# Optimization experiments

Hardware: AMD Instinct MI355X
Metric: run time of the kernel (lower is better)

Reference implementation:

```python
import jax, jax.numpy as jnp
import numpy as np

N_NODES = 100000
N_REL = 4
N_EDGES = 400000
IN_F, H_F, OUT_F = 128, 128, 64


def setup_inputs() -> dict:
    key = jax.random.key(0)
    ks = jax.random.split(key, 7)
    x = jax.random.normal(ks[0], (N_NODES, IN_F), dtype=jnp.float32)
    src_idx = jax.random.randint(ks[1], (N_REL, N_EDGES), 0, N_NODES, dtype=jnp.int64)
    dst_idx = jax.random.randint(ks[2], (N_REL, N_EDGES), 0, N_NODES, dtype=jnp.int64)
    # Glorot-ish scale for the per-relation GraphConv weights
    W1 = jax.random.normal(ks[3], (N_REL, IN_F, H_F), dtype=jnp.float32) * (1.0 / np.sqrt(IN_F))
    b1 = jnp.zeros((N_REL, H_F), dtype=jnp.float32)
    W2 = jax.random.normal(ks[4], (N_REL, H_F, OUT_F), dtype=jnp.float32) * (1.0 / np.sqrt(H_F))
    b2 = jnp.zeros((N_REL, OUT_F), dtype=jnp.float32)
    return {"x": x, "src_idx": src_idx, "dst_idx": dst_idx,
            "W1": W1, "b1": b1, "W2": W2, "b2": b2}


def _graph_conv(x, src, dst, W, b):
    """DGL GraphConv with norm='both': out = D_in^{-1/2} A^T D_out^{-1/2} x W + b."""
    n = x.shape[0]
    ones = jnp.ones(src.shape[0], dtype=x.dtype)
    deg_out = jnp.maximum(jax.ops.segment_sum(ones, src, num_segments=n), 1.0)
    deg_in = jnp.maximum(jax.ops.segment_sum(ones, dst, num_segments=n), 1.0)
    xn = x * jax.lax.rsqrt(deg_out)[:, None]              # [N, F] src-side norm
    msg = jnp.take(xn, src, axis=0)                        # [E, F] gather
    agg = jax.ops.segment_sum(msg, dst, num_segments=n)   # [N, F] scatter-add
    agg = agg * jax.lax.rsqrt(deg_in)[:, None]            # dst-side norm
    return agg @ W + b


def _hetero_layer(x, src_idx, dst_idx, Ws, bs):
    # per-relation conv, sum-aggregated across relations (HeteroGraphConv 'sum')
    per_rel = jax.vmap(lambda s, d, W, b: _graph_conv(x, s, d, W, b))(src_idx, dst_idx, Ws, bs)
    return per_rel.sum(axis=0)


def reference(x, src_idx, dst_idx, W1, b1, W2, b2):
    h = jax.nn.relu(_hetero_layer(x, src_idx, dst_idx, W1, b1))
    return _hetero_layer(h, src_idx, dst_idx, W2, b2)
```

## Files before the change

kernel.cpp:

```cpp
#include <hip/hip_runtime.h>
#include <hip/hip_bf16.h>

#define NN 100000
#define NR 4
#define NE 400000
#define INF 128
#define HF 128
#define OUTF 64

#define WIN 16384
#define WIN2 (WIN / 2)
#define NWIN 7
#define SUB 16
#define SLICE (NE / SUB)

typedef __attribute__((ext_vector_type(8))) short s16x8;
typedef __attribute__((ext_vector_type(4))) float f32x4;

__global__ __launch_bounds__(256) void deg_win_kernel(const int* __restrict__ src,
                                                      const int* __restrict__ dst,
                                                      unsigned int* __restrict__ parts) {
    __shared__ unsigned int hist[WIN2];
    int arr = blockIdx.z;
    int r   = blockIdx.y;
    int win = blockIdx.x / SUB;
    int sub = blockIdx.x % SUB;
    const int4* idx4 = (const int4*)((arr ? dst : src) + (size_t)r * NE + (size_t)sub * SLICE);
    int base = win * WIN;

    uint4 z4 = make_uint4(0, 0, 0, 0);
    for (int i = threadIdx.x; i < WIN2 / 4; i += 256) ((uint4*)hist)[i] = z4;
    __syncthreads();

    auto proc = [&](int4 v) {
        int a;
        a = v.x - base; if ((unsigned)a < WIN) atomicAdd(&hist[a >> 1], 1u << ((a & 1) << 4));
        a = v.y - base; if ((unsigned)a < WIN) atomicAdd(&hist[a >> 1], 1u << ((a & 1) << 4));
        a = v.z - base; if ((unsigned)a < WIN) atomicAdd(&hist[a >> 1], 1u << ((a & 1) << 4));
        a = v.w - base; if ((unsigned)a < WIN) atomicAdd(&hist[a >> 1], 1u << ((a & 1) << 4));
    };

    constexpr int NV = SLICE / 4;
    int i = threadIdx.x;
    for (; i + 256 < NV; i += 512) {
        int4 va = idx4[i];
        int4 vb = idx4[i + 256];
        proc(va);
        proc(vb);
    }
    if (i < NV) proc(idx4[i]);
    __syncthreads();

    unsigned int* outp = parts + ((((size_t)arr * NR + r) * NWIN + win) * SUB + sub) * WIN2;
    for (int j = threadIdx.x; j < WIN2 / 4; j += 256)
        ((uint4*)outp)[j] = ((const uint4*)hist)[j];
}

__global__ void red_norm_kernel(const unsigned int* __restrict__ parts, int* __restrict__ deg_tot,
                                float* __restrict__ rno, float* __restrict__ rni) {
    int n = blockIdx.x * blockDim.x + threadIdx.x;
    if (n >= NN) return;
    int win = n / WIN, off = n % WIN;
    int word = off >> 1, sh = (off & 1) << 4;
    int tot = 0;
    #pragma unroll
    for (int r = 0; r < NR; r++) {
        const unsigned int* p0 = parts + (((size_t)0 * NR + r) * NWIN + win) * SUB * WIN2 + word;
        const unsigned int* p1 = parts + (((size_t)1 * NR + r) * NWIN + win) * SUB * WIN2 + word;
        int so = 0, si = 0;
        #pragma unroll
        for (int s = 0; s < SUB; s++) {
            so += (p0[(size_t)s * WIN2] >> sh) & 0xFFFFu;
            si += (p1[(size_t)s * WIN2] >> sh) & 0xFFFFu;
        }
        rno[(size_t)r * NN + n] = rsqrtf(fmaxf((float)so, 1.0f));
        rni[(size_t)r * NN + n] = rsqrtf(fmaxf((float)si, 1.0f));
        tot += si;
    }
    deg_tot[n] = tot;
}

__global__ void scan_block_kernel(const int* __restrict__ in, int* __restrict__ out,
                                  int* __restrict__ blockSums, int n) {
    __shared__ int sd[256];
    int t = threadIdx.x;
    int base = blockIdx.x * 1024 + t * 4;
    int v[4];
    #pragma unroll
    for (int j = 0; j < 4; j++) v[j] = (base + j < n) ? in[base + j] : 0;
    int ts = v[0] + v[1] + v[2] + v[3];
    sd[t] = ts;
    __syncthreads();
    int acc = ts;
    for (int off = 1; off < 256; off <<= 1) {
        int x = (t >= off) ? sd[t - off] : 0;
        __syncthreads();
        acc += x; sd[t] = acc;
        __syncthreads();
    }
    int run = acc - ts;
    #pragma unroll
    for (int j = 0; j < 4; j++) {
        if (base + j < n) out[base + j] = run;
        run += v[j];
    }
    if (t == 255) blockSums[blockIdx.x] = acc;
}

__global__ void scan_sums_kernel(int* __restrict__ blockSums, int nb) {
    __shared__ int sd[512];
    int t = threadIdx.x;
    int v = (t < nb) ? blockSums[t] : 0;
    sd[t] = v;
    __syncthreads();
    int acc = v;
    for (int off = 1; off < 512; off <<= 1) {
        int x = (t >= off) ? sd[t - off] : 0;
        __syncthreads();
        acc += x; sd[t] = acc;
        __syncthreads();
    }
    if (t < nb) blockSums[t] = acc - v;
}

__global__ void scan_add_kernel(int* __restrict__ row_ptr, const int* __restrict__ blockSums,
                                int* __restrict__ cursor, int n) {
    int i = blockIdx.x * blockDim.x + threadIdx.x;
    if (i < n) {
        int v = row_ptr[i] + blockSums[i >> 10];
        row_ptr[i] = v;
        cursor[i] = v;
    }
    if (i == 0) row_ptr[n] = NR * NE;
}

__global__ void csr_build_kernel(const int* __restrict__ src, const int* __restrict__ dst,
                                 const float* __restrict__ rno, const float* __restrict__ rni,
                                 int* __restrict__ cursor, int2* __restrict__ edges) {
    int r = blockIdx.y;
    int i = blockIdx.x * blockDim.x + threadIdx.x;
    if (i >= NE) return;
    int s = src[(size_t)r * NE + i];
    int d = dst[(size_t)r * NE + i];
    int pos = atomicAdd(&cursor[d], 1);
    float c = rno[(size_t)r * NN + s] * rni[(size_t)r * NN + d];
    edges[pos] = make_int2(r * NN + s, __float_as_int(c));
}

__global__ void bsum_kernel(const float* __restrict__ b1, const float* __restrict__ b2,
                            float* __restrict__ bsum1, float* __restrict__ bsum2) {
    int t = threadIdx.x;
    if (t < HF) {
        float s = 0.f;
        for (int r = 0; r < NR; r++) s += b1[r * HF + t];
        bsum1[t] = s;
    } else if (t < HF + OUTF) {
        int f = t - HF;
        float s = 0.f;
        for (int r = 0; r < NR; r++) s += b2[r * OUTF + f];
        bsum2[f] = s;
    }
}

__global__ void conv_w_kernel(const float* __restrict__ W1, const float* __restrict__ W2,
                              __hip_bfloat16* __restrict__ Wt1, __hip_bfloat16* __restrict__ Wt2) {
    int id = blockIdx.x * blockDim.x + threadIdx.x;
    if (id < NR * HF * INF) {
        int r = id >> 14, rem = id & 16383;
        int n_ = rem >> 7, k = rem & 127;
        Wt1[id] = __float2bfloat16(W1[((size_t)r * INF + k) * HF + n_]);
    } else {
        int id2 = id - NR * HF * INF;
        if (id2 < NR * OUTF * HF) {
            int r = id2 >> 13, rem = id2 & 8191;
            int n_ = rem >> 7, k = rem & 127;
            Wt2[id2] = __float2bfloat16(W2[((size_t)r * HF + k) * OUTF + n_]);
        }
    }
}

__device__ __forceinline__ s16x8 pack_bf16x8(float4 a0, float4 a1) {
    union { s16x8 v; __hip_bfloat162 h[4]; } u;
    u.h[0] = __float22bfloat162_rn(make_float2(a0.x, a0.y));
    u.h[1] = __float22bfloat162_rn(make_float2(a0.z, a0.w));
    u.h[2] = __float22bfloat162_rn(make_float2(a1.x, a1.y));
    u.h[3] = __float22bfloat162_rn(make_float2(a1.z, a1.w));
    return u.v;
}

__device__ __forceinline__ void load_lds_16(const void* g, void* l) {
    __builtin_amdgcn_global_load_lds(
        (const __attribute__((address_space(1))) void*)g,
        (__attribute__((address_space(3))) void*)l, 16, 0, 0);
}

template<int F, typename AT>
__global__ __launch_bounds__(256, 3) void gemm_all(const AT* __restrict__ Xb,
                                                   const __hip_bfloat16* __restrict__ Wt,
                                                   __hip_bfloat16* __restrict__ Zb, int nrel) {
    constexpr int NT = F / 16;
    constexpr int NG = F * 16;
    __shared__ __attribute__((aligned(16))) __hip_bfloat16 Bs[F * 128];

    int tid  = threadIdx.x;
    int wid  = tid >> 6;
    int lane = tid & 63;
    int quad = lane >> 4;
    int l16  = lane & 15;
    int sw   = l16 & 7;

    int mbase = blockIdx.x * 128;

    int bofs[4];
    #pragma unroll
    for (int kb = 0; kb < 4; kb++)
        bofs[kb] = l16 * 256 + (((kb * 4 + quad) ^ sw) << 4);

    s16x8 afr[2][4];
    #pragma unroll
    for (int mt = 0; mt < 2; mt++) {
        int mrow = mbase + mt * 64 + wid * 16 + l16;
        if (mrow >= NN) mrow = NN - 1;
        #pragma unroll
        for (int kb = 0; kb < 4; kb++) {
            if constexpr (sizeof(AT) == 4) {
                const float* xr = (const float*)Xb + (size_t)mrow * 128 + kb * 32 + quad * 8;
                float4 a0 = *(const float4*)xr;
                float4 a1 = *(const float4*)(xr + 4);
                afr[mt][kb] = pack_bf16x8(a0, a1);
            } else {
                afr[mt][kb] = *(const s16x8*)((const __hip_bfloat16*)Xb + (size_t)mrow * 128 + kb * 32 + quad * 8);
            }
        }
    }

    for (int rel = 0; rel < nrel; rel++) {
        if (rel) __syncthreads();

        {
            const char* W = (const char*)(Wt + (size_t)rel * F * 128);
            #pragma unroll
            for (int it = 0; it < NG / 256; it++) {
                int dg = it * 256 + tid;
                int sg = dg ^ ((dg >> 4) & 7);
                load_lds_16(W + (size_t)sg * 16, (char*)Bs + (size_t)(dg & ~63) * 16);
            }
        }
        __syncthreads();

        __hip_bfloat16* Z = Zb + (size_t)rel * NN * F;

        f32x4 acc[2][NT];
        #pragma unroll
        for (int nt = 0; nt < NT; nt++) {
            acc[0][nt] = (f32x4){0.f, 0.f, 0.f, 0.f};
            acc[1][nt] = (f32x4){0.f, 0.f, 0.f, 0.f};
            #pragma unroll
            for (int kb = 0; kb < 4; kb++) {
                s16x8 bfr = *(const s16x8*)((const char*)Bs + nt * 4096 + bofs[kb]);
                acc[0][nt] = __builtin_amdgcn_mfma_f32_16x16x32_bf16(bfr, afr[0][kb], acc[0][nt], 0, 0, 0);
                acc[1][nt] = __builtin_amdgcn_mfma_f32_16x16x32_bf16(bfr, afr[1][kb], acc[1][nt], 0, 0, 0);
            }
        }

        #pragma unroll
        for (int mt = 0; mt < 2; mt++) {
            int g = mbase + mt * 64 + wid * 16 + l16;
            if (g < NN) {
                #pragma unroll
                for (int nt = 0; nt < NT; nt++) {
                    union { uint2 u; __hip_bfloat162 h[2]; } o;
                    o.h[0] = __float22bfloat162_rn(make_float2(acc[mt][nt][0], acc[mt][nt][1]));
                    o.h[1] = __float22bfloat162_rn(make_float2(acc[mt][nt][2], acc[mt][nt][3]));
                    *(uint2*)(Z + (size_t)g * F + nt * 16 + quad * 4) = o.u;
                }
            }
        }
    }
}

template<int F, bool RELU, bool OUT_F32>
__global__ void gather_merged(const int* __restrict__ row_ptr, const int2* __restrict__ edges,
                              const __hip_bfloat16* __restrict__ Zb,
                              float* __restrict__ outf, __hip_bfloat16* __restrict__ outb,
                              const float* __restrict__ bsum) {
    int wid  = threadIdx.x >> 6;
    int lane = threadIdx.x & 63;
    int n = blockIdx.x * (blockDim.x >> 6) + wid;
    if (n >= NN) return;
    int beg = row_ptr[n];
    int end = row_ptr[n + 1];

    if constexpr (F == 128) {
        float2 a = *(const float2*)(bsum + lane * 2);
        for (int p = beg; p < end; p += 8) {
            int   ss[8]; float cc[8];
            #pragma unroll
            for (int j = 0; j < 8; j++) {
                int q = (p + j < end) ? p + j : end - 1;
                int2 e = edges[q];
                ss[j] = e.x;
                cc[j] = (p + j < end) ? __int_as_float(e.y) : 0.f;
            }
            float2 zz[8];
            #pragma unroll
            for (int j = 0; j < 8; j++)
                zz[j] = __bfloat1622float2(*(const __hip_bfloat162*)(Zb + (size_t)ss[j] * 128 + lane * 2));
            #pragma unroll
            for (int j = 0; j < 8; j++) {
                a.x = fmaf(cc[j], zz[j].x, a.x);
                a.y = fmaf(cc[j], zz[j].y, a.y);
            }
        }
        if constexpr (RELU) { a.x = fmaxf(a.x, 0.f); a.y = fmaxf(a.y, 0.f); }
        *(__hip_bfloat162*)(outb + (size_t)n * 128 + lane * 2) = __float22bfloat162_rn(a);
    } else {
        float a = bsum[lane];
        for (int p = beg; p < end; p += 8) {
            int   ss[8]; float cc[8];
            #pragma unroll
            for (int j = 0; j < 8; j++) {
                int q = (p + j < end) ? p + j : end - 1;
                int2 e = edges[q];
                ss[j] = e.x;
                cc[j] = (p + j < end) ? __int_as_float(e.y) : 0.f;
            }
            float zz[8];
            #pragma unroll
            for (int j = 0; j < 8; j++)
                zz[j] = __bfloat162float(Zb[(size_t)ss[j] * 64 + lane]);
            #pragma unroll
            for (int j = 0; j < 8; j++) a = fmaf(cc[j], zz[j], a);
        }
        if constexpr (RELU) a = fmaxf(a, 0.f);
        if constexpr (OUT_F32) outf[(size_t)n * 64 + lane] = a;
        else outb[(size_t)n * 64 + lane] = __float2bfloat16(a);
    }
}

extern "C" void kernel_launch(void* const* d_in, const int* in_sizes, int n_in,
                              void* d_out, int out_size, void* d_ws, size_t ws_size,
                              hipStream_t stream) {
    const float* x   = (const float*)d_in[0];
    const int*   src = (const int*)  d_in[1];
    const int*   dst = (const int*)  d_in[2];
    const float* W1  = (const float*)d_in[3];
    const float* b1  = (const float*)d_in[4];
    const float* W2  = (const float*)d_in[5];
    const float* b2  = (const float*)d_in[6];
    float* out = (float*)d_out;

    constexpr int RN = NR * NN;
    constexpr int NB = (NN + 1023) / 1024;

    char* p = (char*)d_ws;
    int*   deg_tot   = (int*)p;   p += (size_t)NN * 4;
    float* rno       = (float*)p; p += (size_t)RN * 4;
    float* rni       = (float*)p; p += (size_t)RN * 4;
    int*   row_ptr   = (int*)p;   p += ((size_t)NN + 16) * 4;
    int*   cursor    = (int*)p;   p += (size_t)NN * 4;
    int*   blockSums = (int*)p;   p += 1024 * 4;
    int2*  edges     = (int2*)p;  p += (size_t)NR * NE * 8;
    float* bsum1 = (float*)p; p += HF * 4;
    float* bsum2 = (float*)p; p += OUTF * 4;
    __hip_bfloat16* hb  = (__hip_bfloat16*)p; p += (size_t)NN * HF * 2;
    __hip_bfloat16* Wt1 = (__hip_bfloat16*)p; p += (size_t)NR * HF * INF * 2;
    __hip_bfloat16* Wt2 = (__hip_bfloat16*)p; p += (size_t)NR * OUTF * HF * 2;
    __hip_bfloat16* Zb = (__hip_bfloat16*)p;
    unsigned int* parts = (unsigned int*)Zb;

    conv_w_kernel<<<(NR * HF * INF + NR * OUTF * HF + 255) / 256, 256, 0, stream>>>(W1, W2, Wt1, Wt2);
    bsum_kernel<<<1, 192, 0, stream>>>(b1, b2, bsum1, bsum2);
    deg_win_kernel<<<dim3(NWIN * SUB, NR, 2), 256, 0, stream>>>(src, dst, parts);
    red_norm_kernel<<<(NN + 255) / 256, 256, 0, stream>>>(parts, deg_tot, rno, rni);
    scan_block_kernel<<<NB, 256, 0, stream>>>(deg_tot, row_ptr, blockSums, NN);
    scan_sums_kernel<<<1, 512, 0, stream>>>(blockSums, NB);
    scan_add_kernel<<<(NN + 255) / 256, 256, 0, stream>>>(row_ptr, blockSums, cursor, NN);
    csr_build_kernel<<<dim3((NE + 255) / 256, NR), 256, 0, stream>>>(
        src, dst, rno, rni, cursor, edges);

    constexpr int GB = (NN + 127) / 128;
    constexpr int GG = (NN + 3) / 4;

    gemm_all<HF, float><<<GB, 256, 0, stream>>>(x, Wt1, Zb, 4);
    gather_merged<HF, true, false><<<GG, 256, 0, stream>>>(
        row_ptr, edges, Zb, nullptr, hb, bsum1);

    gemm_all<OUTF, __hip_bfloat16><<<GB, 256, 0, stream>>>(hb, Wt2, Zb, 4);
    gather_merged<OUTF, false, true><<<GG, 256, 0, stream>>>(
        row_ptr, edges, Zb, out, nullptr, bsum2);
}
```

Baseline: 453.2 us.

## Aggregate before transform using per-relation CSR and fused GEMM epilogue

Reorders each hetero layer to gather neighbor features per (node, relation) key first, then apply the per-relation weights in a single GEMM that accumulates across relations and adds bias/ReLU. The CSR is rebuilt keyed by node*4+relation, and x is pre-converted to bf16. This avoids writing and randomly gathering the per-relation transformed Z tensor, but gathers 128-wide rows in layer 2 and writes a 4x intermediate aggregate.

```diff
diff --git a/kernel.cpp b/kernel.cpp
--- a/kernel.cpp
+++ b/kernel.cpp
@@ -56,13 +56,12 @@
         ((uint4*)outp)[j] = ((const uint4*)hist)[j];
 }
 
-__global__ void red_norm_kernel(const unsigned int* __restrict__ parts, int* __restrict__ deg_tot,
+__global__ void red_norm_kernel(const unsigned int* __restrict__ parts, int* __restrict__ deg4,
                                 float* __restrict__ rno, float* __restrict__ rni) {
     int n = blockIdx.x * blockDim.x + threadIdx.x;
     if (n >= NN) return;
     int win = n / WIN, off = n % WIN;
     int word = off >> 1, sh = (off & 1) << 4;
-    int tot = 0;
     #pragma unroll
     for (int r = 0; r < NR; r++) {
         const unsigned int* p0 = parts + (((size_t)0 * NR + r) * NWIN + win) * SUB * WIN2 + word;
@@ -75,9 +74,8 @@
         }
         rno[(size_t)r * NN + n] = rsqrtf(fmaxf((float)so, 1.0f));
         rni[(size_t)r * NN + n] = rsqrtf(fmaxf((float)si, 1.0f));
-        tot += si;
-    }
-    deg_tot[n] = tot;
+        deg4[n * 4 + r] = si;
+    }
 }
 
 __global__ void scan_block_kernel(const int* __restrict__ in, int* __restrict__ out,
@@ -142,9 +140,9 @@
     if (i >= NE) return;
     int s = src[(size_t)r * NE + i];
     int d = dst[(size_t)r * NE + i];
-    int pos = atomicAdd(&cursor[d], 1);
+    int pos = atomicAdd(&cursor[d * 4 + r], 1);
     float c = rno[(size_t)r * NN + s] * rni[(size_t)r * NN + d];
-    edges[pos] = make_int2(r * NN + s, __float_as_int(c));
+    edges[pos] = make_int2(s, __float_as_int(c));
 }
 
 __global__ void bsum_kernel(const float* __restrict__ b1, const float* __restrict__ b2,
@@ -188,16 +186,60 @@
     return u.v;
 }
 
+__global__ __launch_bounds__(256) void xb_kernel(const float* __restrict__ x,
+                                                 __hip_bfloat16* __restrict__ xb) {
+    int i = blockIdx.x * 256 + threadIdx.x;
+    const float4* xp = (const float4*)x + (size_t)i * 2;
+    float4 a0 = xp[0], a1 = xp[1];
+    *(s16x8*)(xb + (size_t)i * 8) = pack_bf16x8(a0, a1);
+}
+
 __device__ __forceinline__ void load_lds_16(const void* g, void* l) {
     __builtin_amdgcn_global_load_lds(
         (const __attribute__((address_space(1))) void*)g,
         (__attribute__((address_space(3))) void*)l, 16, 0, 0);
 }
 
-template<int F, typename AT>
-__global__ __launch_bounds__(256, 3) void gemm_all(const AT* __restrict__ Xb,
+__global__ __launch_bounds__(256) void gather_agg(const int* __restrict__ row_ptr4,
+                                                  const int2* __restrict__ edges,
+                                                  const __hip_bfloat16* __restrict__ Xb,
+                                                  __hip_bfloat16* __restrict__ aggb) {
+    int wid  = threadIdx.x >> 6;
+    int lane = threadIdx.x & 63;
+    int key  = blockIdx.x * 4 + wid;
+    int beg = row_ptr4[key];
+    int end = row_ptr4[key + 1];
+    float2 a = make_float2(0.f, 0.f);
+    for (int p = beg; p < end; p += 8) {
+        int m = end - p;
+        int2 e[8];
+        #pragma unroll
+        for (int j = 0; j < 8; j++) {
+            int q = (j < m) ? p + j : end - 1;
+            e[j] = edges[q];
+        }
+        float2 zz[8];
+        #pragma unroll
+        for (int j = 0; j < 8; j++)
+            if (j < m)
+                zz[j] = __bfloat1622float2(*(const __hip_bfloat162*)(Xb + (size_t)e[j].x * 128 + lane * 2));
+        #pragma unroll
+        for (int j = 0; j < 8; j++)
+            if (j < m) {
+                float c = __int_as_float(e[j].y);
+                a.x = fmaf(c, zz[j].x, a.x);
+                a.y = fmaf(c, zz[j].y, a.y);
+            }
+    }
+    *(__hip_bfloat162*)(aggb + (size_t)key * 128 + lane * 2) = __float22bfloat162_rn(a);
+}
+
+template<int F, bool RELU, bool OUT_F32>
+__global__ __launch_bounds__(256, 3) void gemm_acc(const __hip_bfloat16* __restrict__ aggb,
                                                    const __hip_bfloat16* __restrict__ Wt,
-                                                   __hip_bfloat16* __restrict__ Zb, int nrel) {
+                                                   float* __restrict__ outf,
+                                                   __hip_bfloat16* __restrict__ outb,
+                                                   const float* __restrict__ bsum) {
     constexpr int NT = F / 16;
     constexpr int NG = F * 16;
     __shared__ __attribute__((aligned(16))) __hip_bfloat16 Bs[F * 128];
@@ -216,27 +258,29 @@
     for (int kb = 0; kb < 4; kb++)
         bofs[kb] = l16 * 256 + (((kb * 4 + quad) ^ sw) << 4);
 
-    s16x8 afr[2][4];
+    int mrow[2];
     #pragma unroll
     for (int mt = 0; mt < 2; mt++) {
-        int mrow = mbase + mt * 64 + wid * 16 + l16;
-        if (mrow >= NN) mrow = NN - 1;
-        #pragma unroll
-        for (int kb = 0; kb < 4; kb++) {
-            if constexpr (sizeof(AT) == 4) {
-                const float* xr = (const float*)Xb + (size_t)mrow * 128 + kb * 32 + quad * 8;
-                float4 a0 = *(const float4*)xr;
-                float4 a1 = *(const float4*)(xr + 4);
-                afr[mt][kb] = pack_bf16x8(a0, a1);
-            } else {
-                afr[mt][kb] = *(const s16x8*)((const __hip_bfloat16*)Xb + (size_t)mrow * 128 + kb * 32 + quad * 8);
-            }
-        }
-    }
-
-    for (int rel = 0; rel < nrel; rel++) {
+        int g = mbase + mt * 64 + wid * 16 + l16;
+        mrow[mt] = (g < NN) ? g : NN - 1;
+    }
+
+    f32x4 acc[2][NT];
+    #pragma unroll
+    for (int nt = 0; nt < NT; nt++) {
+        acc[0][nt] = (f32x4){0.f, 0.f, 0.f, 0.f};
+        acc[1][nt] = (f32x4){0.f, 0.f, 0.f, 0.f};
+    }
+
+    for (int rel = 0; rel < NR; rel++) {
+        s16x8 afr[2][4];
+        #pragma unroll
+        for (int mt = 0; mt < 2; mt++)
+            #pragma unroll
+            for (int kb = 0; kb < 4; kb++)
+                afr[mt][kb] = *(const s16x8*)(aggb + ((size_t)mrow[mt] * 4 + rel) * 128 + kb * 32 + quad * 8);
+
         if (rel) __syncthreads();
-
         {
             const char* W = (const char*)(Wt + (size_t)rel * F * 128);
             #pragma unroll
@@ -248,13 +292,8 @@
         }
         __syncthreads();
 
-        __hip_bfloat16* Z = Zb + (size_t)rel * NN * F;
-
-        f32x4 acc[2][NT];
         #pragma unroll
         for (int nt = 0; nt < NT; nt++) {
-            acc[0][nt] = (f32x4){0.f, 0.f, 0.f, 0.f};
-            acc[1][nt] = (f32x4){0.f, 0.f, 0.f, 0.f};
             #pragma unroll
             for (int kb = 0; kb < 4; kb++) {
                 s16x8 bfr = *(const s16x8*)((const char*)Bs + nt * 4096 + bofs[kb]);
@@ -262,79 +301,33 @@
                 acc[1][nt] = __builtin_amdgcn_mfma_f32_16x16x32_bf16(bfr, afr[1][kb], acc[1][nt], 0, 0, 0);
             }
         }
-
-        #pragma unroll
-        for (int mt = 0; mt < 2; mt++) {
-            int g = mbase + mt * 64 + wid * 16 + l16;
-            if (g < NN) {
-                #pragma unroll
-                for (int nt = 0; nt < NT; nt++) {
+    }
+
+    #pragma unroll
+    for (int mt = 0; mt < 2; mt++) {
+        int g = mbase + mt * 64 + wid * 16 + l16;
+        if (g < NN) {
+            #pragma unroll
+            for (int nt = 0; nt < NT; nt++) {
+                float4 bb = *(const float4*)(bsum + nt * 16 + quad * 4);
+                float v0 = acc[mt][nt][0] + bb.x;
+                float v1 = acc[mt][nt][1] + bb.y;
+                float v2 = acc[mt][nt][2] + bb.z;
+                float v3 = acc[mt][nt][3] + bb.w;
+                if constexpr (RELU) {
+                    v0 = fmaxf(v0, 0.f); v1 = fmaxf(v1, 0.f);
+                    v2 = fmaxf(v2, 0.f); v3 = fmaxf(v3, 0.f);
+                }
+                if constexpr (OUT_F32) {
+                    *(float4*)(outf + (size_t)g * F + nt * 16 + quad * 4) = make_float4(v0, v1, v2, v3);
+                } else {
                     union { uint2 u; __hip_bfloat162 h[2]; } o;
-                    o.h[0] = __float22bfloat162_rn(make_float2(acc[mt][nt][0], acc[mt][nt][1]));
-                    o.h[1] = __float22bfloat162_rn(make_float2(acc[mt][nt][2], acc[mt][nt][3]));
-                    *(uint2*)(Z + (size_t)g * F + nt * 16 + quad * 4) = o.u;
+                    o.h[0] = __float22bfloat162_rn(make_float2(v0, v1));
+                    o.h[1] = __float22bfloat162_rn(make_float2(v2, v3));
+                    *(uint2*)(outb + (size_t)g * F + nt * 16 + quad * 4) = o.u;
                 }
             }
         }
-    }
-}
-
-template<int F, bool RELU, bool OUT_F32>
-__global__ void gather_merged(const int* __restrict__ row_ptr, const int2* __restrict__ edges,
-                              const __hip_bfloat16* __restrict__ Zb,
-                              float* __restrict__ outf, __hip_bfloat16* __restrict__ outb,
-                              const float* __restrict__ bsum) {
-    int wid  = threadIdx.x >> 6;
-    int lane = threadIdx.x & 63;
-    int n = blockIdx.x * (blockDim.x >> 6) + wid;
-    if (n >= NN) return;
-    int beg = row_ptr[n];
-    int end = row_ptr[n + 1];
-
-    if constexpr (F == 128) {
-        float2 a = *(const float2*)(bsum + lane * 2);
-        for (int p = beg; p < end; p += 8) {
-            int   ss[8]; float cc[8];
-            #pragma unroll
-            for (int j = 0; j < 8; j++) {
-                int q = (p + j < end) ? p + j : end - 1;
-                int2 e = edges[q];
-                ss[j] = e.x;
-                cc[j] = (p + j < end) ? __int_as_float(e.y) : 0.f;
-            }
-            float2 zz[8];
-            #pragma unroll
-            for (int j = 0; j < 8; j++)
-                zz[j] = __bfloat1622float2(*(const __hip_bfloat162*)(Zb + (size_t)ss[j] * 128 + lane * 2));
-            #pragma unroll
-            for (int j = 0; j < 8; j++) {
-                a.x = fmaf(cc[j], zz[j].x, a.x);
-                a.y = fmaf(cc[j], zz[j].y, a.y);
-            }
-        }
-        if constexpr (RELU) { a.x = fmaxf(a.x, 0.f); a.y = fmaxf(a.y, 0.f); }
-        *(__hip_bfloat162*)(outb + (size_t)n * 128 + lane * 2) = __float22bfloat162_rn(a);
-    } else {
-        float a = bsum[lane];
-        for (int p = beg; p < end; p += 8) {
-            int   ss[8]; float cc[8];
-            #pragma unroll
-            for (int j = 0; j < 8; j++) {
-                int q = (p + j < end) ? p + j : end - 1;
-                int2 e = edges[q];
-                ss[j] = e.x;
-                cc[j] = (p + j < end) ? __int_as_float(e.y) : 0.f;
-            }
-            float zz[8];
-            #pragma unroll
-            for (int j = 0; j < 8; j++)
-                zz[j] = __bfloat162float(Zb[(size_t)ss[j] * 64 + lane]);
-            #pragma unroll
-            for (int j = 0; j < 8; j++) a = fmaf(cc[j], zz[j], a);
-        }
-        if constexpr (RELU) a = fmaxf(a, 0.f);
-        if constexpr (OUT_F32) outf[(size_t)n * 64 + lane] = a;
-        else outb[(size_t)n * 64 + lane] = __float2bfloat16(a);
     }
 }
 
@@ -350,43 +343,43 @@
     const float* b2  = (const float*)d_in[6];
     float* out = (float*)d_out;
 
-    constexpr int RN = NR * NN;
-    constexpr int NB = (NN + 1023) / 1024;
+    constexpr int RN  = NR * NN;
+    constexpr int NB4 = (RN + 1023) / 1024;
 
     char* p = (char*)d_ws;
-    int*   deg_tot   = (int*)p;   p += (size_t)NN * 4;
+    int*   deg4      = (int*)p;   p += (size_t)RN * 4;
     float* rno       = (float*)p; p += (size_t)RN * 4;
     float* rni       = (float*)p; p += (size_t)RN * 4;
-    int*   row_ptr   = (int*)p;   p += ((size_t)NN + 16) * 4;
-    int*   cursor    = (int*)p;   p += (size_t)NN * 4;
+    int*   row_ptr4  = (int*)p;   p += ((size_t)RN + 16) * 4;
+    int*   cursor4   = (int*)p;   p += (size_t)RN * 4;
     int*   blockSums = (int*)p;   p += 1024 * 4;
     int2*  edges     = (int2*)p;  p += (size_t)NR * NE * 8;
     float* bsum1 = (float*)p; p += HF * 4;
     float* bsum2 = (float*)p; p += OUTF * 4;
+    __hip_bfloat16* xb  = (__hip_bfloat16*)p; p += (size_t)NN * INF * 2;
     __hip_bfloat16* hb  = (__hip_bfloat16*)p; p += (size_t)NN * HF * 2;
     __hip_bfloat16* Wt1 = (__hip_bfloat16*)p; p += (size_t)NR * HF * INF * 2;
     __hip_bfloat16* Wt2 = (__hip_bfloat16*)p; p += (size_t)NR * OUTF * HF * 2;
-    __hip_bfloat16* Zb = (__hip_bfloat16*)p;
-    unsigned int* parts = (unsigned int*)Zb;
+    __hip_bfloat16* aggb = (__hip_bfloat16*)p;
+    unsigned int* parts = (unsigned int*)aggb;
 
     conv_w_kernel<<<(NR * HF * INF + NR * OUTF * HF + 255) / 256, 256, 0, stream>>>(W1, W2, Wt1, Wt2);
+    xb_kernel<<<NN * INF / 8 / 256, 256, 0, stream>>>(x, xb);
     bsum_kernel<<<1, 192, 0, stream>>>(b1, b2, bsum1, bsum2);
+
     deg_win_kernel<<<dim3(NWIN * SUB, NR, 2), 256, 0, stream>>>(src, dst, parts);
-    red_norm_kernel<<<(NN + 255) / 256, 256, 0, stream>>>(parts, deg_tot, rno, rni);
-    scan_block_kernel<<<NB, 256, 0, stream>>>(deg_tot, row_ptr, blockSums, NN);
-    scan_sums_kernel<<<1, 512, 0, stream>>>(blockSums, NB);
-    scan_add_kernel<<<(NN + 255) / 256, 256, 0, stream>>>(row_ptr, blockSums, cursor, NN);
+    red_norm_kernel<<<(NN + 255) / 256, 256, 0, stream>>>(parts, deg4, rno, rni);
+    scan_block_kernel<<<NB4, 256, 0, stream>>>(deg4, row_ptr4, blockSums, RN);
+    scan_sums_kernel<<<1, 512, 0, stream>>>(blockSums, NB4);
+    scan_add_kernel<<<(RN + 255) / 256, 256, 0, stream>>>(row_ptr4, blockSums, cursor4, RN);
     csr_build_kernel<<<dim3((NE + 255) / 256, NR), 256, 0, stream>>>(
-        src, dst, rno, rni, cursor, edges);
+        src, dst, rno, rni, cursor4, edges);
 
     constexpr int GB = (NN + 127) / 128;
-    constexpr int GG = (NN + 3) / 4;
-
-    gemm_all<HF, float><<<GB, 256, 0, stream>>>(x, Wt1, Zb, 4);
-    gather_merged<HF, true, false><<<GG, 256, 0, stream>>>(
-        row_ptr, edges, Zb, nullptr, hb, bsum1);
-
-    gemm_all<OUTF, __hip_bfloat16><<<GB, 256, 0, stream>>>(hb, Wt2, Zb, 4);
-    gather_merged<OUTF, false, true><<<GG, 256, 0, stream>>>(
-        row_ptr, edges, Zb, out, nullptr, bsum2);
-}
+
+    gather_agg<<<NN, 256, 0, stream>>>(row_ptr4, edges, xb, aggb);
+    gemm_acc<HF, true, false><<<GB, 256, 0, stream>>>(aggb, Wt1, nullptr, hb, bsum1);
+
+    gather_agg<<<NN, 256, 0, stream>>>(row_ptr4, edges, hb, aggb);
+    gemm_acc<OUTF, false, true><<<GB, 256, 0, stream>>>(aggb, Wt2, out, nullptr, bsum2);
+}
```

After: 644.9 us. +42.3%, slower.

## Pad CSR rows to multiples of eight and pre-shift gather offsets

Applied to the files above, without the earlier changes.

Each node's CSR row is rounded up to a multiple of 8 edges and the padding slots are filled with zero-weight dummy edges. This lets the gather kernels drop per-edge bounds checks and clamping. Source indices are stored pre-shifted by 8 so the gather computes byte offsets directly, and the node bounds check is removed because NN is divisible by 4. The weight-conversion and bias-sum kernels are merged into one launch. The cost is extra padded edges (up to 7 per node), an added pad-fill kernel, and a 32-bit shifted index that must not overflow.

```diff
diff --git a/kernel.cpp b/kernel.cpp
--- a/kernel.cpp
+++ b/kernel.cpp
@@ -60,6 +60,7 @@
                                 float* __restrict__ rno, float* __restrict__ rni) {
     int n = blockIdx.x * blockDim.x + threadIdx.x;
     if (n >= NN) return;
+    if (n == 0) deg_tot[NN] = 0;
     int win = n / WIN, off = n % WIN;
     int word = off >> 1, sh = (off & 1) << 4;
     int tot = 0;
@@ -87,7 +88,7 @@
     int base = blockIdx.x * 1024 + t * 4;
     int v[4];
     #pragma unroll
-    for (int j = 0; j < 4; j++) v[j] = (base + j < n) ? in[base + j] : 0;
+    for (int j = 0; j < 4; j++) v[j] = (base + j < n) ? ((in[base + j] + 7) & ~7) : 0;
     int ts = v[0] + v[1] + v[2] + v[3];
     sd[t] = ts;
     __syncthreads();
@@ -129,9 +130,17 @@
     if (i < n) {
         int v = row_ptr[i] + blockSums[i >> 10];
         row_ptr[i] = v;
-        cursor[i] = v;
-    }
-    if (i == 0) row_ptr[n] = NR * NE;
+        if (i < NN) cursor[i] = v;
+    }
+}
+
+__global__ void pad_fill_kernel(const int* __restrict__ row_ptr, const int* __restrict__ deg_tot,
+                                int2* __restrict__ edges) {
+    int n = blockIdx.x * blockDim.x + threadIdx.x;
+    if (n >= NN) return;
+    int b = row_ptr[n] + deg_tot[n];
+    int e = row_ptr[n + 1];
+    for (int i = b; i < e; i++) edges[i] = make_int2(0, 0);
 }
 
 __global__ void csr_build_kernel(const int* __restrict__ src, const int* __restrict__ dst,
@@ -144,27 +153,28 @@
     int d = dst[(size_t)r * NE + i];
     int pos = atomicAdd(&cursor[d], 1);
     float c = rno[(size_t)r * NN + s] * rni[(size_t)r * NN + d];
-    edges[pos] = make_int2(r * NN + s, __float_as_int(c));
-}
-
-__global__ void bsum_kernel(const float* __restrict__ b1, const float* __restrict__ b2,
+    edges[pos] = make_int2((r * NN + s) << 8, __float_as_int(c));
+}
+
+__global__ void prep_kernel(const float* __restrict__ W1, const float* __restrict__ W2,
+                            const float* __restrict__ b1, const float* __restrict__ b2,
+                            __hip_bfloat16* __restrict__ Wt1, __hip_bfloat16* __restrict__ Wt2,
                             float* __restrict__ bsum1, float* __restrict__ bsum2) {
-    int t = threadIdx.x;
-    if (t < HF) {
-        float s = 0.f;
-        for (int r = 0; r < NR; r++) s += b1[r * HF + t];
-        bsum1[t] = s;
-    } else if (t < HF + OUTF) {
-        int f = t - HF;
-        float s = 0.f;
-        for (int r = 0; r < NR; r++) s += b2[r * OUTF + f];
-        bsum2[f] = s;
-    }
-}
-
-__global__ void conv_w_kernel(const float* __restrict__ W1, const float* __restrict__ W2,
-                              __hip_bfloat16* __restrict__ Wt1, __hip_bfloat16* __restrict__ Wt2) {
-    int id = blockIdx.x * blockDim.x + threadIdx.x;
+    if (blockIdx.x == 384) {
+        int t = threadIdx.x;
+        if (t < HF) {
+            float s = 0.f;
+            for (int r = 0; r < NR; r++) s += b1[r * HF + t];
+            bsum1[t] = s;
+        } else if (t < HF + OUTF) {
+            int f = t - HF;
+            float s = 0.f;
+            for (int r = 0; r < NR; r++) s += b2[r * OUTF + f];
+            bsum2[f] = s;
+        }
+        return;
+    }
+    int id = blockIdx.x * 256 + threadIdx.x;
     if (id < NR * HF * INF) {
         int r = id >> 14, rem = id & 16383;
         int n_ = rem >> 7, k = rem & 127;
@@ -280,57 +290,50 @@
 }
 
 template<int F, bool RELU, bool OUT_F32>
-__global__ void gather_merged(const int* __restrict__ row_ptr, const int2* __restrict__ edges,
+__global__ __launch_bounds__(256) void gather_merged(const int* __restrict__ row_ptr,
+                              const int2* __restrict__ edges,
                               const __hip_bfloat16* __restrict__ Zb,
                               float* __restrict__ outf, __hip_bfloat16* __restrict__ outb,
                               const float* __restrict__ bsum) {
     int wid  = threadIdx.x >> 6;
     int lane = threadIdx.x & 63;
-    int n = blockIdx.x * (blockDim.x >> 6) + wid;
-    if (n >= NN) return;
+    int n = blockIdx.x * 4 + wid;
     int beg = row_ptr[n];
     int end = row_ptr[n + 1];
 
     if constexpr (F == 128) {
+        const char* Zl = (const char*)Zb + lane * 4;
         float2 a = *(const float2*)(bsum + lane * 2);
         for (int p = beg; p < end; p += 8) {
-            int   ss[8]; float cc[8];
+            int2 e[8];
+            #pragma unroll
+            for (int j = 0; j < 8; j++) e[j] = edges[p + j];
+            float2 zz[8];
+            #pragma unroll
+            for (int j = 0; j < 8; j++)
+                zz[j] = __bfloat1622float2(*(const __hip_bfloat162*)(Zl + e[j].x));
             #pragma unroll
             for (int j = 0; j < 8; j++) {
-                int q = (p + j < end) ? p + j : end - 1;
-                int2 e = edges[q];
-                ss[j] = e.x;
-                cc[j] = (p + j < end) ? __int_as_float(e.y) : 0.f;
-            }
-            float2 zz[8];
-            #pragma unroll
-            for (int j = 0; j < 8; j++)
-                zz[j] = __bfloat1622float2(*(const __hip_bfloat162*)(Zb + (size_t)ss[j] * 128 + lane * 2));
-            #pragma unroll
-            for (int j = 0; j < 8; j++) {
-                a.x = fmaf(cc[j], zz[j].x, a.x);
-                a.y = fmaf(cc[j], zz[j].y, a.y);
+                float c = __int_as_float(e[j].y);
+                a.x = fmaf(c, zz[j].x, a.x);
+                a.y = fmaf(c, zz[j].y, a.y);
             }
         }
         if constexpr (RELU) { a.x = fmaxf(a.x, 0.f); a.y = fmaxf(a.y, 0.f); }
         *(__hip_bfloat162*)(outb + (size_t)n * 128 + lane * 2) = __float22bfloat162_rn(a);
     } else {
+        const char* Zl = (const char*)Zb + lane * 2;
         float a = bsum[lane];
         for (int p = beg; p < end; p += 8) {
-            int   ss[8]; float cc[8];
-            #pragma unroll
-            for (int j = 0; j < 8; j++) {
-                int q = (p + j < end) ? p + j : end - 1;
-                int2 e = edges[q];
-                ss[j] = e.x;
-                cc[j] = (p + j < end) ? __int_as_float(e.y) : 0.f;
-            }
+            int2 e[8];
+            #pragma unroll
+            for (int j = 0; j < 8; j++) e[j] = edges[p + j];
             float zz[8];
             #pragma unroll
             for (int j = 0; j < 8; j++)
-                zz[j] = __bfloat162float(Zb[(size_t)ss[j] * 64 + lane]);
-            #pragma unroll
-            for (int j = 0; j < 8; j++) a = fmaf(cc[j], zz[j], a);
+                zz[j] = __bfloat162float(*(const __hip_bfloat16*)(Zl + (e[j].x >> 1)));
+            #pragma unroll
+            for (int j = 0; j < 8; j++) a = fmaf(__int_as_float(e[j].y), zz[j], a);
         }
         if constexpr (RELU) a = fmaxf(a, 0.f);
         if constexpr (OUT_F32) outf[(size_t)n * 64 + lane] = a;
@@ -351,16 +354,17 @@
     float* out = (float*)d_out;
 
     constexpr int RN = NR * NN;
-    constexpr int NB = (NN + 1023) / 1024;
+    constexpr int NSC = NN + 1;
+    constexpr int NB = (NSC + 1023) / 1024;
 
     char* p = (char*)d_ws;
-    int*   deg_tot   = (int*)p;   p += (size_t)NN * 4;
+    int*   deg_tot   = (int*)p;   p += ((size_t)NN + 16) * 4;
     float* rno       = (float*)p; p += (size_t)RN * 4;
     float* rni       = (float*)p; p += (size_t)RN * 4;
     int*   row_ptr   = (int*)p;   p += ((size_t)NN + 16) * 4;
     int*   cursor    = (int*)p;   p += (size_t)NN * 4;
     int*   blockSums = (int*)p;   p += 1024 * 4;
-    int2*  edges     = (int2*)p;  p += (size_t)NR * NE * 8;
+    int2*  edges     = (int2*)p;  p += ((size_t)NR * NE + 8 * NN) * 8;
     float* bsum1 = (float*)p; p += HF * 4;
     float* bsum2 = (float*)p; p += OUTF * 4;
     __hip_bfloat16* hb  = (__hip_bfloat16*)p; p += (size_t)NN * HF * 2;
@@ -369,18 +373,18 @@
     __hip_bfloat16* Zb = (__hip_bfloat16*)p;
     unsigned int* parts = (unsigned int*)Zb;
 
-    conv_w_kernel<<<(NR * HF * INF + NR * OUTF * HF + 255) / 256, 256, 0, stream>>>(W1, W2, Wt1, Wt2);
-    bsum_kernel<<<1, 192, 0, stream>>>(b1, b2, bsum1, bsum2);
+    prep_kernel<<<385, 256, 0, stream>>>(W1, W2, b1, b2, Wt1, Wt2, bsum1, bsum2);
     deg_win_kernel<<<dim3(NWIN * SUB, NR, 2), 256, 0, stream>>>(src, dst, parts);
     red_norm_kernel<<<(NN + 255) / 256, 256, 0, stream>>>(parts, deg_tot, rno, rni);
-    scan_block_kernel<<<NB, 256, 0, stream>>>(deg_tot, row_ptr, blockSums, NN);
+    scan_block_kernel<<<NB, 256, 0, stream>>>(deg_tot, row_ptr, blockSums, NSC);
     scan_sums_kernel<<<1, 512, 0, stream>>>(blockSums, NB);
-    scan_add_kernel<<<(NN + 255) / 256, 256, 0, stream>>>(row_ptr, blockSums, cursor, NN);
+    scan_add_kernel<<<(NSC + 255) / 256, 256, 0, stream>>>(row_ptr, blockSums, cursor, NSC);
+    pad_fill_kernel<<<(NN + 255) / 256, 256, 0, stream>>>(row_ptr, deg_tot, edges);
     csr_build_kernel<<<dim3((NE + 255) / 256, NR), 256, 0, stream>>>(
         src, dst, rno, rni, cursor, edges);
 
     constexpr int GB = (NN + 127) / 128;
-    constexpr int GG = (NN + 3) / 4;
+    constexpr int GG = NN / 4;
 
     gemm_all<HF, float><<<GB, 256, 0, stream>>>(x, Wt1, Zb, 4);
     gather_merged<HF, true, false><<<GG, 256, 0, stream>>>(
```

Measured after the change: 400.2 us. 1.13x faster.
